# Kernel optimization log

Measured on AMD Instinct MI355X. Metric: run time of the kernel, lower is better.

## Reference

```python
import jax, jax.numpy as jnp
import numpy as np

B = 32; NMAX = 256; E = 512; H = 512; U = 256; M = 32; L = 2; P = 4; TAU = 1.0
S = NMAX + 1                      # pseudo-seq len = nodes + SOS
IN0 = E + (M - 1) + P             # GRU layer-0 input size


def setup_inputs() -> dict:
    key = jax.random.key(0)
    ks = jax.random.split(key, 22)
    f = lambda k, sh, sc=0.05: jax.random.normal(k, sh, dtype=jnp.float32) * sc
    return {
        "h_padded": jax.random.normal(ks[0], (B, NMAX, E), jnp.float32),
        "hg": jax.random.normal(ks[1], (B, E), jnp.float32),
        "num_nodes": jax.random.randint(ks[2], (B,), 1, NMAX + 1),
        "u_noise": jax.random.uniform(ks[3], (M, B, S), jnp.float32),
        "emb_special": f(ks[4], (2, E), 1.0),
        "emb_pos": f(ks[5], (M, P), 1.0),
        "Wp": f(ks[6], (L * H, E)), "bp": f(ks[7], (L * H,)),
        "W_ih0": f(ks[8], (3 * H, IN0)), "W_hh0": f(ks[9], (3 * H, H)),
        "b_ih0": f(ks[10], (3 * H,)), "b_hh0": f(ks[11], (3 * H,)),
        "W_ih1": f(ks[12], (3 * H, H)), "W_hh1": f(ks[13], (3 * H, H)),
        "b_ih1": f(ks[14], (3 * H,)), "b_hh1": f(ks[15], (3 * H,)),
        "W1": f(ks[16], (U, H)), "W2": f(ks[17], (U, H)),
        "wc": f(ks[18], (U,)), "V": f(ks[19], (U,)),
        "Wf": f(ks[20], (M - 1, H)), "bf": f(ks[21], (M - 1,)),
    }


def _gru_step(x, hid, params):
    # torch nn.GRU single time step, L layers; gate order (r, z, n)
    new = []
    inp = x
    for l, (Wi, Wh, bi, bh) in enumerate(params):
        hp = hid[l]
        gi = inp @ Wi.T + bi
        gh = hp @ Wh.T + bh
        gi_r, gi_z, gi_n = jnp.split(gi, 3, axis=-1)
        gh_r, gh_z, gh_n = jnp.split(gh, 3, axis=-1)
        r = jax.nn.sigmoid(gi_r + gh_r)
        z = jax.nn.sigmoid(gi_z + gh_z)
        n = jnp.tanh(gi_n + r * gh_n)
        hn = (1.0 - z) * n + z * hp
        new.append(hn)
        inp = hn
    return inp, jnp.stack(new, 0)


def reference(h_padded, hg, num_nodes, u_noise, emb_special, emb_pos, Wp, bp,
              W_ih0, W_hh0, b_ih0, b_hh0, W_ih1, W_hh1, b_ih1, b_hh1,
              W1, W2, wc, V, Wf, bf):
    lens = num_nodes + 1
    mask = jnp.arange(S)[None, :] < lens[:, None]                       # [B,S]
    node_valid = (jnp.arange(NMAX)[None, :] < num_nodes[:, None]).astype(h_padded.dtype)
    # encoder_out = [SOS emb ; h nodes ; zero pad] as pad_sequence would give
    sos_enc = jnp.broadcast_to(emb_special[1], (B, 1, E))
    encoder_out = jnp.concatenate([sos_enc, h_padded * node_valid[..., None]], axis=1)  # [B,S,E]
    enc_W1 = encoder_out @ W1.T                                          # [B,S,U] hoisted (loop-invariant)
    dec_hidden = jnp.tanh(hg @ Wp.T + bp).reshape(B, L, H).transpose(1, 0, 2)  # [L,B,H]
    theta0 = jnp.zeros((B, M - 1), encoder_out.dtype)
    dec_input = jnp.concatenate([jnp.broadcast_to(emb_special[0], (B, E)), theta0], axis=1)
    cov_vec0 = jnp.zeros((B, S), encoder_out.dtype)
    gumbel = -jnp.log(-jnp.log(u_noise + 1e-10) + 1e-10)                 # [M,B,S]
    gru_params = ((W_ih0, W_hh0, b_ih0, b_hh0), (W_ih1, W_hh1, b_ih1, b_hh1))
    neg = jnp.float32(-1e30)

    def step(carry, xs):
        dec_in, hid, cov_vec, cov_loss = carry
        i, pe, g = xs
        x = jnp.concatenate([dec_in, jnp.broadcast_to(pe, (B, P))], axis=1)
        out, hid = _gru_step(x, hid, gru_params)                        # out [B,H]
        # Bahdanau attention with coverage
        uj = enc_W1 + (out @ W2.T)[:, None, :] + cov_vec[..., None] * wc
        uj = jnp.tanh(uj) @ V                                           # [B,S]
        aj = jax.nn.softmax(jnp.where(mask, uj, neg), axis=-1)
        # hard gumbel-softmax (straight-through)
        logits = jnp.log(aj + 1e-12)
        y = jax.nn.softmax((logits + g) / TAU, axis=1)
        onehot = jax.nn.one_hot(jnp.argmax(y, axis=1), S, dtype=y.dtype)
        hard = jax.lax.stop_gradient(onehot - y) + y
        chosen = jnp.einsum('bse,bs->be', encoder_out, hard)            # [B,E]
        cov_loss = cov_loss + jnp.minimum(aj, cov_vec).sum()
        cov_vec = cov_vec + aj
        theta = jnp.where(i < 1,
                          jnp.zeros((B, M - 1), out.dtype),
                          jax.nn.sigmoid(out @ Wf.T + bf))
        dec_next = jnp.concatenate([chosen, theta], axis=1)
        return (dec_next, hid, cov_vec, cov_loss), (hard, theta, aj)

    init = (dec_input, dec_hidden, cov_vec0, jnp.float32(0.0))
    xs = (jnp.arange(M), emb_pos, gumbel)
    carry_f, (hards, thetas, ajs) = jax.lax.scan(step, init, xs)
    cov_loss = carry_f[3] / B
    pointer = jnp.transpose(hards, (1, 2, 0))   # [B,S,M]
    adj = jnp.transpose(thetas, (1, 2, 0))      # [B,M-1,M]
    atts = jnp.transpose(ajs, (1, 2, 0))        # [B,S,M]
    return pointer, cov_loss, encoder_out, adj, atts
```

## Files before the change

kernel.cpp:

```cpp
#include <hip/hip_runtime.h>

constexpr int NB  = 32;
constexpr int NMX = 256;
constexpr int ED  = 512;
constexpr int HD  = 512;
constexpr int UD  = 256;
constexpr int MS  = 32;
constexpr int PD  = 4;
constexpr int SD  = 257;
constexpr int IL0 = 547;
constexpr int XP  = 576;

constexpr long long OFF_PTR  = 0;
constexpr long long OFF_COVL = (long long)NB*SD*MS;
constexpr long long OFF_ENC  = OFF_COVL + 1;
constexpr long long OFF_ADJ  = OFF_ENC + (long long)NB*SD*ED;
constexpr long long OFF_ATT  = OFF_ADJ + (long long)NB*(MS-1)*MS;

__device__ __forceinline__ float sigf(float x){ return 1.0f/(1.0f + __expf(-x)); }
__device__ __forceinline__ float ftanh(float x){ float e = __expf(2.0f*x); return 1.0f - 2.0f/(e + 1.0f); }

__global__ __launch_bounds__(256) void k_pro(const float* __restrict__ hp,
    const float* __restrict__ hg, const float* __restrict__ embsp,
    const float* __restrict__ embpos, const float* __restrict__ W1,
    const float* __restrict__ Wih0, const float* __restrict__ W2,
    const int* __restrict__ nn, const float4* __restrict__ Wp4,
    const float* __restrict__ bp,
    float* __restrict__ out, float* __restrict__ encA, int useA,
    float4* __restrict__ encW1,
    float* __restrict__ x4, float* __restrict__ cov, float* __restrict__ covl,
    float* __restrict__ Wih0_4, float* __restrict__ W2T,
    float* __restrict__ h0, float* __restrict__ h1){
  __shared__ __align__(16) float As[16][68];
  __shared__ __align__(16) float Bs[16][68];
  int blk = blockIdx.x, t = threadIdx.x;
  if (blk < 516){
    int bm = blk >> 2, bn = blk & 3;
    int m0 = bm*64, n0 = bn*64;
    int tm = t >> 4, tn = t & 15;
    float4 acc[4];
    #pragma unroll
    for (int i = 0; i < 4; ++i) acc[i] = {0.f,0.f,0.f,0.f};
    int arow = t >> 2, akq = t & 3;
    int r = m0 + arow;
    int amode = 0;
    const float* abase = embsp + ED;
    if (r < NB*SD){
      int ab = r / SD, as = r - ab*SD;
      if (as == 0) amode = 1;
      else if (as <= nn[ab]){ amode = 2; abase = hp + ((long long)ab*NMX + (as-1))*ED; }
    }
    int bk = t & 15, bu = t >> 4;
    for (int k0 = 0; k0 < 512; k0 += 16){
      float4 av = {0.f,0.f,0.f,0.f};
      if (amode) av = *(const float4*)(abase + k0 + akq*4);
      float bv[4];
      #pragma unroll
      for (int j = 0; j < 4; ++j)
        bv[j] = W1[(long long)(n0 + bu*4 + j)*ED + k0 + bk];
      __syncthreads();
      As[akq*4 + 0][arow] = av.x;
      As[akq*4 + 1][arow] = av.y;
      As[akq*4 + 2][arow] = av.z;
      As[akq*4 + 3][arow] = av.w;
      *(float4*)&Bs[bk][bu*4] = make_float4(bv[0], bv[1], bv[2], bv[3]);
      __syncthreads();
      #pragma unroll
      for (int kk = 0; kk < 16; ++kk){
        float4 a = *(const float4*)&As[kk][tm*4];
        float4 bq = *(const float4*)&Bs[kk][tn*4];
        acc[0].x += a.x*bq.x; acc[0].y += a.x*bq.y; acc[0].z += a.x*bq.z; acc[0].w += a.x*bq.w;
        acc[1].x += a.y*bq.x; acc[1].y += a.y*bq.y; acc[1].z += a.y*bq.z; acc[1].w += a.y*bq.w;
        acc[2].x += a.z*bq.x; acc[2].y += a.z*bq.y; acc[2].z += a.z*bq.z; acc[2].w += a.z*bq.w;
        acc[3].x += a.w*bq.x; acc[3].y += a.w*bq.y; acc[3].z += a.w*bq.z; acc[3].w += a.w*bq.w;
      }
    }
    #pragma unroll
    for (int i = 0; i < 4; ++i){
      int rr = m0 + tm*4 + i;
      if (rr < NB*SD) encW1[(long long)rr*64 + (n0 >> 2) + tn] = acc[i];
    }
  } else if (blk < 644){
    int b = t & 31;
    int row = (blk - 516)*8 + (t >> 5);
    const float4* w = Wp4 + (long long)row*128;
    const float4* xg = (const float4*)(hg + (long long)b*ED);
    float acc = bp[row];
    #pragma unroll 4
    for (int i = 0; i < 128; ++i){
      float4 wv = w[i], xv = xg[i];
      acc += wv.x*xv.x + wv.y*xv.y + wv.z*xv.z + wv.w*xv.w;
    }
    float v = ftanh(acc);
    int h = row & 511;
    int idx = (h >> 2)*128 + b*4 + (h & 3);
    if (row < HD) h0[idx] = v;
    else          h1[idx] = v;
  } else {
    int eb = blk - 644;
    {
      int r = eb*2 + (t >> 7);
      int tid = t & 127;
      int b = r / SD, s = r - b*SD;
      float4 v = {0.f,0.f,0.f,0.f};
      if (s == 0) v = *(const float4*)(embsp + ED + tid*4);
      else if (s <= nn[b]) v = *(const float4*)(hp + ((long long)b*NMX + (s-1))*ED + tid*4);
      float* dst = out + OFF_ENC + (long long)r*ED + tid*4;
      dst[0] = v.x; dst[1] = v.y; dst[2] = v.z; dst[3] = v.w;
      if (useA) *(float4*)(encA + (long long)r*ED + tid*4) = v;
    }
    const int N0 = XP*NB;
    const int N1 = N0 + NB*SD;
    const int N2 = N1 + NB;
    const int N3 = N2 + 1536*XP;
    const int N4 = N3 + ED*UD;
    for (int i = eb*256 + t; i < N4; i += 4112*256){
      if (i < N0){
        int kb = i >> 7, rr = i & 3;
        int k = kb*4 + rr;
        float v;
        if (k < ED) v = embsp[k];
        else if (k < ED + MS - 1) v = 0.f;
        else if (k < IL0) v = embpos[k - (ED + MS - 1)];
        else v = 0.f;
        x4[i] = v;
      } else if (i < N1){
        cov[i - N0] = 0.f;
      } else if (i < N2){
        covl[i - N1] = 0.f;
      } else if (i < N3){
        int j = i - N2; int row = j / XP, c = j % XP;
        Wih0_4[j] = (c < IL0) ? Wih0[(long long)row*IL0 + c] : 0.f;
      } else {
        int j = i - N3; int k = j / UD, u = j % UD;
        W2T[j] = W2[(long long)u*HD + k];
      }
    }
  }
}

__device__ __forceinline__ void hh_pre(const float4* __restrict__ h4,
    const float4* __restrict__ Whh4, float* __restrict__ ghh,
    int bh, int t, float (*part)[NB][8][6]){
  int b = t & 31, ks = (t >> 5) & 7, hl = (t >> 8) & 1;
  int h = bh*2 + hl;
  float a0 = 0.f, a1 = 0.f, a2 = 0.f;
  const float4* w0 = Whh4 + (long long)(0*HD + h)*128 + ks*16;
  const float4* w1 = Whh4 + (long long)(1*HD + h)*128 + ks*16;
  const float4* w2 = Whh4 + (long long)(2*HD + h)*128 + ks*16;
  const float4* hb = h4 + (long long)(ks*16)*NB + b;
  #pragma unroll
  for (int kb = 0; kb < 16; ++kb){
    float4 xv = hb[kb*NB];
    float4 a = w0[kb], c = w1[kb], d = w2[kb];
    a0 += xv.x*a.x + xv.y*a.y + xv.z*a.z + xv.w*a.w;
    a1 += xv.x*c.x + xv.y*c.y + xv.z*c.z + xv.w*c.w;
    a2 += xv.x*d.x + xv.y*d.y + xv.z*d.z + xv.w*d.w;
  }
  part[hl][b][ks][0] = a0; part[hl][b][ks][1] = a1; part[hl][b][ks][2] = a2;
  __syncthreads();
  if (t < 64){
    int b2 = t & 31, hl2 = t >> 5;
    int h2 = bh*2 + hl2;
    float g0 = 0.f, g1 = 0.f, g2 = 0.f;
    #pragma unroll
    for (int k = 0; k < 8; ++k){
      g0 += part[hl2][b2][k][0]; g1 += part[hl2][b2][k][1]; g2 += part[hl2][b2][k][2];
    }
    ghh[(0*HD + h2)*NB + b2] = g0;
    ghh[(1*HD + h2)*NB + b2] = g1;
    ghh[(2*HD + h2)*NB + b2] = g2;
  }
}

template<int PER, bool PRE>
__global__ __launch_bounds__(512) void k_gru(const float4* __restrict__ x4,
                      const float4* __restrict__ h4,
                      const float4* __restrict__ Wih4, const float4* __restrict__ Whh4,
                      const float* __restrict__ bih, const float* __restrict__ bhh,
                      float* __restrict__ outT, const float* __restrict__ ghh){
  constexpr int NI4 = PER*8;
  __shared__ float part[2][NB][8][6];
  int t = threadIdx.x;
  int b = t & 31, ks = (t >> 5) & 7, hl = (t >> 8) & 1;
  int h = blockIdx.x*2 + hl;
  float ai0 = 0.f, ai1 = 0.f, ai2 = 0.f;
  {
    const float4* w0 = Wih4 + (long long)(0*HD + h)*NI4 + ks*PER;
    const float4* w1 = Wih4 + (long long)(1*HD + h)*NI4 + ks*PER;
    const float4* w2 = Wih4 + (long long)(2*HD + h)*NI4 + ks*PER;
    const float4* xb = x4 + (long long)(ks*PER)*NB + b;
    #pragma unroll
    for (int kb = 0; kb < PER; ++kb){
      float4 xv = xb[kb*NB];
      float4 a = w0[kb], c = w1[kb], d = w2[kb];
      ai0 += xv.x*a.x + xv.y*a.y + xv.z*a.z + xv.w*a.w;
      ai1 += xv.x*c.x + xv.y*c.y + xv.z*c.z + xv.w*c.w;
      ai2 += xv.x*d.x + xv.y*d.y + xv.z*d.z + xv.w*d.w;
    }
  }
  if (!PRE){
    float ah0 = 0.f, ah1 = 0.f, ah2 = 0.f;
    const float4* w0 = Whh4 + (long long)(0*HD + h)*128 + ks*16;
    const float4* w1 = Whh4 + (long long)(1*HD + h)*128 + ks*16;
    const float4* w2 = Whh4 + (long long)(2*HD + h)*128 + ks*16;
    const float4* hb = h4 + (long long)(ks*16)*NB + b;
    #pragma unroll
    for (int kb = 0; kb < 16; ++kb){
      float4 xv = hb[kb*NB];
      float4 a = w0[kb], c = w1[kb], d = w2[kb];
      ah0 += xv.x*a.x + xv.y*a.y + xv.z*a.z + xv.w*a.w;
      ah1 += xv.x*c.x + xv.y*c.y + xv.z*c.z + xv.w*c.w;
      ah2 += xv.x*d.x + xv.y*d.y + xv.z*d.z + xv.w*d.w;
    }
    part[hl][b][ks][3] = ah0; part[hl][b][ks][4] = ah1; part[hl][b][ks][5] = ah2;
  }
  part[hl][b][ks][0] = ai0; part[hl][b][ks][1] = ai1; part[hl][b][ks][2] = ai2;
  __syncthreads();
  if (t < 64){
    int b2 = t & 31, hl2 = t >> 5;
    int h2 = blockIdx.x*2 + hl2;
    float g0=0.f,g1=0.f,g2=0.f;
    #pragma unroll
    for (int k = 0; k < 8; ++k){
      g0 += part[hl2][b2][k][0]; g1 += part[hl2][b2][k][1]; g2 += part[hl2][b2][k][2];
    }
    float ghr, ghz, ghn;
    if (PRE){
      ghr = ghh[(0*HD + h2)*NB + b2];
      ghz = ghh[(1*HD + h2)*NB + b2];
      ghn = ghh[(2*HD + h2)*NB + b2];
    } else {
      float g3=0.f,g4=0.f,g5=0.f;
      #pragma unroll
      for (int k = 0; k < 8; ++k){
        g3 += part[hl2][b2][k][3]; g4 += part[hl2][b2][k][4]; g5 += part[hl2][b2][k][5];
      }
      ghr = g3; ghz = g4; ghn = g5;
    }
    float gir = g0 + bih[h2], giz = g1 + bih[HD + h2], gin = g2 + bih[2*HD + h2];
    ghr += bhh[h2]; ghz += bhh[HD + h2]; ghn += bhh[2*HD + h2];
    float r = sigf(gir + ghr);
    float z = sigf(giz + ghz);
    float nn = ftanh(gin + r*ghn);
    int idx = (h2 >> 2)*128 + b2*4 + (h2 & 3);
    float hp = ((const float*)h4)[idx];
    outT[idx] = (1.f - z)*nn + z*hp;
  }
}

__global__ __launch_bounds__(512) void k_qs(const float4* __restrict__ h1,
                      const float4* __restrict__ W2T4, const float4* __restrict__ Wf4,
                      const float* __restrict__ bfv, const float* __restrict__ embpos,
                      int m, const float4* __restrict__ encW1,
                      const float4* __restrict__ wc4, const float4* __restrict__ V4,
                      const int* __restrict__ nn,
                      const float* __restrict__ cov, float* __restrict__ sc,
                      float* __restrict__ x4, float* __restrict__ out,
                      const float4* __restrict__ Whh1_4, float* __restrict__ ghh1){
  union QMem {
    struct { float h1s[512]; float wcs[256]; float Vs[256]; float qs[256];
             float4 qpart[8][64]; } q;
    float part[2][NB][8][6];
  };
  __shared__ __align__(16) QMem sm;
  int t = threadIdx.x;
  if (blockIdx.x >= 256){
    hh_pre(h1, Whh1_4, ghh1, blockIdx.x - 256, t, sm.part);
    return;
  }
  int b = blockIdx.x >> 3, seg = blockIdx.x & 7;
  int n = nn[b];
  if (seg != 0 && seg*33 > n) return;
  if (t < 128) ((float4*)sm.q.h1s)[t] = h1[t*NB + b];
  else if (t < 192) ((float4*)sm.q.wcs)[t - 128] = wc4[t - 128];
  else if (t < 256) ((float4*)sm.q.Vs)[t - 192] = V4[t - 192];
  __syncthreads();
  {
    int u4 = t & 63, kq = t >> 6;
    float4 acc = {0.f,0.f,0.f,0.f};
    const float4* w = W2T4 + (long long)(kq*64)*64 + u4;
    const float* hh = sm.q.h1s + kq*64;
    #pragma unroll 4
    for (int k = 0; k < 64; ++k){
      float a = hh[k];
      float4 wv = w[(long long)k*64];
      acc.x += a*wv.x; acc.y += a*wv.y; acc.z += a*wv.z; acc.w += a*wv.w;
    }
    sm.q.qpart[kq][u4] = acc;
  }
  __syncthreads();
  if (t < 64){
    float4 s = sm.q.qpart[0][t];
    #pragma unroll
    for (int k = 1; k < 8; ++k){
      float4 p = sm.q.qpart[k][t];
      s.x += p.x; s.y += p.y; s.z += p.z; s.w += p.w;
    }
    ((float4*)sm.q.qs)[t] = s;
  } else if (seg == 0){
    int w = (t >> 6) - 1;
    int lane = t & 63;
    for (int j = w; j < MS-1; j += 7){
      const float4* wf = Wf4 + (long long)j*128 + lane*2;
      float4 w0 = wf[0], w1v = wf[1];
      const float4* hh4 = (const float4*)sm.q.h1s + lane*2;
      float4 hv0 = hh4[0], hv1 = hh4[1];
      float d = w0.x*hv0.x + w0.y*hv0.y + w0.z*hv0.z + w0.w*hv0.w
              + w1v.x*hv1.x + w1v.y*hv1.y + w1v.z*hv1.z + w1v.w*hv1.w;
      for (int off = 32; off; off >>= 1) d += __shfl_xor(d, off);
      if (lane == 0){
        float th = (m < 1) ? 0.f : sigf(d + bfv[j]);
        out[OFF_ADJ + (long long)b*(MS-1)*MS + (long long)j*MS + m] = th;
        int k = ED + j;
        x4[(k >> 2)*128 + b*4 + (k & 3)] = th;
      }
    }
  }
  if (seg == 0 && t == 0 && m + 1 < MS){
    #pragma unroll
    for (int p = 0; p < PD; ++p){
      int k = ED + MS - 1 + p;
      x4[(k >> 2)*128 + b*4 + (k & 3)] = embpos[(m+1)*PD + p];
    }
  }
  __syncthreads();
  int lane = t & 63, wav = t >> 6;
  int s0 = seg*33;
  float4 q4 = ((const float4*)sm.q.qs)[lane];
  float4 wv = ((const float4*)sm.q.wcs)[lane];
  float4 vv = ((const float4*)sm.q.Vs)[lane];
  for (int s = s0 + wav; s < s0 + 33 && s < SD; s += 8){
    if (s > n) continue;
    float cv = cov[b*SD + s];
    float4 e4 = encW1[((long long)b*SD + s)*64 + lane];
    float acc = vv.x*ftanh(e4.x + q4.x + cv*wv.x)
              + vv.y*ftanh(e4.y + q4.y + cv*wv.y)
              + vv.z*ftanh(e4.z + q4.z + cv*wv.z)
              + vv.w*ftanh(e4.w + q4.w + cv*wv.w);
    for (int off = 32; off; off >>= 1) acc += __shfl_xor(acc, off);
    if (lane == 0) sc[b*SD + s] = acc;
  }
}

__global__ __launch_bounds__(512) void k_soft(const float* __restrict__ sc,
                      const int* __restrict__ nn, const float* __restrict__ un, int m,
                      float* __restrict__ cov, float* __restrict__ covl,
                      float* __restrict__ out, float4* __restrict__ x4,
                      const float* __restrict__ encSrc, int alignedA,
                      const float4* __restrict__ h0n4,
                      const float4* __restrict__ Whh0_4, float* __restrict__ ghh0){
  union SMem {
    struct { float red[8]; float redc[8]; int redi[8]; float s_mx, s_den; int s_k; } s;
    float part[2][NB][8][6];
  };
  __shared__ __align__(16) SMem sm;
  int t = threadIdx.x;
  if (blockIdx.x >= 32){
    hh_pre(h0n4, Whh0_4, ghh0, blockIdx.x - 32, t, sm.part);
    return;
  }
  int b = blockIdx.x;
  int lane = t & 63, wav = t >> 6;
  int n = nn[b];
  float sv = (t < SD) ? sc[b*SD + t] : -3.4e38f;
  float cv = (t < SD) ? cov[b*SD + t] : 0.f;
  float v1 = (t < SD && t <= n) ? sv : -3.4e38f;
  for (int off = 32; off; off >>= 1) v1 = fmaxf(v1, __shfl_xor(v1, off));
  if (lane == 0) sm.s.red[wav] = v1;
  __syncthreads();
  if (t == 0){
    float mm = sm.s.red[0];
    for (int i = 1; i < 8; ++i) mm = fmaxf(mm, sm.s.red[i]);
    sm.s.s_mx = mm;
  }
  __syncthreads();
  float ev = (t < SD && t <= n) ? __expf(sv - sm.s.s_mx) : 0.f;
  float v2 = ev;
  for (int off = 32; off; off >>= 1) v2 += __shfl_xor(v2, off);
  if (lane == 0) sm.s.red[wav] = v2;
  __syncthreads();
  if (t == 0){
    float ss = 0.f;
    for (int i = 0; i < 8; ++i) ss += sm.s.red[i];
    sm.s.s_den = ss;
  }
  __syncthreads();
  float aj = (t < SD) ? ev / sm.s.s_den : 0.f;
  float yl = -3.4e38f; int idx = SD; float lcl = 0.f;
  if (t < SD){
    float u = un[((long long)m*NB + b)*SD + t];
    float g = -__logf(-__logf(u + 1e-10f) + 1e-10f);
    yl = __logf(aj + 1e-12f) + g;
    idx = t;
    lcl = fminf(aj, cv);
    cov[b*SD + t] = cv + aj;
    out[OFF_ATT + ((long long)b*SD + t)*MS + m] = aj;
  }
  for (int off = 32; off; off >>= 1){
    float oy = __shfl_xor(yl, off); int oi = __shfl_xor(idx, off);
    if (oy > yl || (oy == yl && oi < idx)){ yl = oy; idx = oi; }
  }
  for (int off = 32; off; off >>= 1) lcl += __shfl_xor(lcl, off);
  if (lane == 0){ sm.s.red[wav] = yl; sm.s.redi[wav] = idx; sm.s.redc[wav] = lcl; }
  __syncthreads();
  if (t == 0){
    float by = sm.s.red[0]; int bi = sm.s.redi[0]; float cl = sm.s.redc[0];
    for (int w = 1; w < 8; ++w){
      if (sm.s.red[w] > by || (sm.s.red[w] == by && sm.s.redi[w] < bi)){
        by = sm.s.red[w]; bi = sm.s.redi[w];
      }
      cl += sm.s.redc[w];
    }
    sm.s.s_k = bi;
    covl[b] += cl;
  }
  __syncthreads();
  int kk = sm.s.s_k;
  if (t < SD) out[OFF_PTR + ((long long)b*SD + t)*MS + m] = (t == kk) ? 1.f : 0.f;
  if (t < 128){
    if (alignedA){
      float4 v = ((const float4*)(encSrc + (long long)(b*SD + kk)*ED))[t];
      x4[t*NB + b] = v;
    } else {
      const float* er = encSrc + (long long)(b*SD + kk)*ED;
      float4 v; v.x = er[t*4]; v.y = er[t*4+1]; v.z = er[t*4+2]; v.w = er[t*4+3];
      x4[t*NB + b] = v;
    }
  }
}

__global__ void k_fin(const float* __restrict__ covl, float* __restrict__ out){
  if (threadIdx.x == 0 && blockIdx.x == 0){
    float s = 0.f;
    for (int i = 0; i < NB; ++i) s += covl[i];
    out[OFF_COVL] = s / (float)NB;
  }
}

extern "C" void kernel_launch(void* const* d_in, const int* in_sizes, int n_in,
                              void* d_out, int out_size, void* d_ws, size_t ws_size,
                              hipStream_t stream){
  const float* h_padded    = (const float*)d_in[0];
  const float* hg          = (const float*)d_in[1];
  const int*   num_nodes   = (const int*)  d_in[2];
  const float* u_noise     = (const float*)d_in[3];
  const float* emb_special = (const float*)d_in[4];
  const float* emb_pos     = (const float*)d_in[5];
  const float* Wp          = (const float*)d_in[6];
  const float* bp          = (const float*)d_in[7];
  const float* W_ih0       = (const float*)d_in[8];
  const float* W_hh0       = (const float*)d_in[9];
  const float* b_ih0       = (const float*)d_in[10];
  const float* b_hh0       = (const float*)d_in[11];
  const float* W_ih1       = (const float*)d_in[12];
  const float* W_hh1       = (const float*)d_in[13];
  const float* b_ih1       = (const float*)d_in[14];
  const float* b_hh1       = (const float*)d_in[15];
  const float* W1          = (const float*)d_in[16];
  const float* W2          = (const float*)d_in[17];
  const float* wc          = (const float*)d_in[18];
  const float* V           = (const float*)d_in[19];
  const float* Wf          = (const float*)d_in[20];
  const float* bf          = (const float*)d_in[21];
  float* out = (float*)d_out;

  float* ws      = (float*)d_ws;
  float* encW1   = ws;  ws += (long long)NB*SD*UD;
  float* Wih0_4  = ws;  ws += (long long)1536*XP;
  float* W2T     = ws;  ws += (long long)UD*ED;
  float* x4      = ws;  ws += XP*NB;
  float* h0      = ws;  ws += 2*HD*NB;
  float* h1      = ws;  ws += 2*HD*NB;
  float* cov     = ws;  ws += NB*SD;
  float* covl    = ws;  ws += NB;
  float* sc      = ws;  ws += NB*SD;
  float* ghh0    = ws;  ws += 3*HD*NB;
  float* ghh1    = ws;  ws += 3*HD*NB;
  float* encA    = ws;
  size_t used_base = (size_t)((char*)ws - (char*)d_ws);
  int useA = (ws_size >= used_base + (size_t)NB*SD*ED*sizeof(float)) ? 1 : 0;
  const float* encSrc = useA ? encA : (out + OFF_ENC);

  k_pro<<<4756, 256, 0, stream>>>(h_padded, hg, emb_special, emb_pos, W1, W_ih0, W2,
                                  num_nodes, (const float4*)Wp, bp, out, encA, useA,
                                  (float4*)encW1, x4, cov, covl, Wih0_4, W2T, h0, h1);

  for (int m = 0; m < MS; ++m){
    float* h0c = h0 + (m & 1)*HD*NB;
    float* h0n = h0 + ((m + 1) & 1)*HD*NB;
    float* h1c = h1 + (m & 1)*HD*NB;
    float* h1n = h1 + ((m + 1) & 1)*HD*NB;
    if (m == 0){
      k_gru<18,false><<<256, 512, 0, stream>>>((const float4*)x4, (const float4*)h0c,
          (const float4*)Wih0_4, (const float4*)W_hh0, b_ih0, b_hh0, h0n, nullptr);
      k_gru<16,false><<<256, 512, 0, stream>>>((const float4*)h0n, (const float4*)h1c,
          (const float4*)W_ih1, (const float4*)W_hh1, b_ih1, b_hh1, h1n, nullptr);
    } else {
      k_gru<18,true><<<256, 512, 0, stream>>>((const float4*)x4, (const float4*)h0c,
          (const float4*)Wih0_4, (const float4*)W_hh0, b_ih0, b_hh0, h0n, ghh0);
      k_gru<16,true><<<256, 512, 0, stream>>>((const float4*)h0n, (const float4*)h1c,
          (const float4*)W_ih1, (const float4*)W_hh1, b_ih1, b_hh1, h1n, ghh1);
    }
    k_qs  <<<512, 512, 0, stream>>>((const float4*)h1n, (const float4*)W2T,
        (const float4*)Wf, bf, emb_pos, m, (const float4*)encW1,
        (const float4*)wc, (const float4*)V, num_nodes, cov, sc, x4, out,
        (const float4*)W_hh1, ghh1);
    k_soft<<<288, 512, 0, stream>>>(sc, num_nodes, u_noise, m, cov, covl, out,
        (float4*)x4, encSrc, useA, (const float4*)h0n, (const float4*)W_hh0, ghh0);
  }
  k_fin<<<1, 64, 0, stream>>>(covl, out);
}
```

Baseline: 1.219 ms.

## Fuse attention scoring and gumbel-softmax into one kernel per decode step

```diff
diff --git a/kernel.cpp b/kernel.cpp
--- a/kernel.cpp
+++ b/kernel.cpp
@@ -28,7 +28,7 @@
     const float* __restrict__ bp,
     float* __restrict__ out, float* __restrict__ encA, int useA,
     float4* __restrict__ encW1,
-    float* __restrict__ x4, float* __restrict__ cov, float* __restrict__ covl,
+    float* __restrict__ x4, float* __restrict__ cov2, float* __restrict__ covp,
     float* __restrict__ Wih0_4, float* __restrict__ W2T,
     float* __restrict__ h0, float* __restrict__ h1){
   __shared__ __align__(16) float As[16][68];
@@ -110,8 +110,8 @@
       if (useA) *(float4*)(encA + (long long)r*ED + tid*4) = v;
     }
     const int N0 = XP*NB;
-    const int N1 = N0 + NB*SD;
-    const int N2 = N1 + NB;
+    const int N1 = N0 + 2*NB*SD;
+    const int N2 = N1 + 256;
     const int N3 = N2 + 1536*XP;
     const int N4 = N3 + ED*UD;
     for (int i = eb*256 + t; i < N4; i += 4112*256){
@@ -125,9 +125,9 @@
         else v = 0.f;
         x4[i] = v;
       } else if (i < N1){
-        cov[i - N0] = 0.f;
+        cov2[i - N0] = 0.f;
       } else if (i < N2){
-        covl[i - N1] = 0.f;
+        covp[i - N1] = 0.f;
       } else if (i < N3){
         int j = i - N2; int row = j / XP, c = j % XP;
         Wih0_4[j] = (c < IL0) ? Wih0[(long long)row*IL0 + c] : 0.f;
@@ -249,62 +249,78 @@
   }
 }
 
-__global__ __launch_bounds__(512) void k_qs(const float4* __restrict__ h1,
+union __align__(16) AMem {
+  struct { __align__(16) float h1s[512]; __align__(16) float wcs[256];
+           __align__(16) float Vs[256];  __align__(16) float qs[256];
+           __align__(16) float4 qpart[8][64]; float scs[SD];
+           float red[8]; float redc[8]; int redi[8];
+           float s_mx, s_den; int s_k; } a;
+  float part[2][NB][8][6];
+};
+
+__global__ __launch_bounds__(512) void k_attn(const float4* __restrict__ h1,
                       const float4* __restrict__ W2T4, const float4* __restrict__ Wf4,
                       const float* __restrict__ bfv, const float* __restrict__ embpos,
                       int m, const float4* __restrict__ encW1,
                       const float4* __restrict__ wc4, const float4* __restrict__ V4,
-                      const int* __restrict__ nn,
-                      const float* __restrict__ cov, float* __restrict__ sc,
-                      float* __restrict__ x4, float* __restrict__ out,
+                      const int* __restrict__ nn, const float* __restrict__ un,
+                      const float* __restrict__ covc, float* __restrict__ covn,
+                      float* __restrict__ covp, float* __restrict__ x4,
+                      float* __restrict__ out, const float* __restrict__ encSrc,
+                      int alignedA,
+                      const float4* __restrict__ h0n4,
+                      const float4* __restrict__ Whh0_4, float* __restrict__ ghh0,
                       const float4* __restrict__ Whh1_4, float* __restrict__ ghh1){
-  union QMem {
-    struct { float h1s[512]; float wcs[256]; float Vs[256]; float qs[256];
-             float4 qpart[8][64]; } q;
-    float part[2][NB][8][6];
-  };
-  __shared__ __align__(16) QMem sm;
+  __shared__ AMem sm;
   int t = threadIdx.x;
-  if (blockIdx.x >= 256){
-    hh_pre(h1, Whh1_4, ghh1, blockIdx.x - 256, t, sm.part);
-    return;
-  }
+  if (blockIdx.x >= 512){ hh_pre(h0n4, Whh0_4, ghh0, blockIdx.x - 512, t, sm.part); return; }
+  if (blockIdx.x >= 256){ hh_pre(h1,   Whh1_4, ghh1, blockIdx.x - 256, t, sm.part); return; }
   int b = blockIdx.x >> 3, seg = blockIdx.x & 7;
   int n = nn[b];
-  if (seg != 0 && seg*33 > n) return;
-  if (t < 128) ((float4*)sm.q.h1s)[t] = h1[t*NB + b];
-  else if (t < 192) ((float4*)sm.q.wcs)[t - 128] = wc4[t - 128];
-  else if (t < 256) ((float4*)sm.q.Vs)[t - 192] = V4[t - 192];
+  int s0 = seg*33;
+  if (seg != 0 && s0 > n){
+    if (t < 33){
+      int s = s0 + t;
+      if (s < SD){
+        out[OFF_ATT + ((long long)b*SD + s)*MS + m] = 0.f;
+        out[OFF_PTR + ((long long)b*SD + s)*MS + m] = 0.f;
+      }
+    }
+    return;
+  }
+  if (t < 128) ((float4*)sm.a.h1s)[t] = h1[t*NB + b];
+  else if (t < 192) ((float4*)sm.a.wcs)[t - 128] = wc4[t - 128];
+  else if (t < 256) ((float4*)sm.a.Vs)[t - 192] = V4[t - 192];
   __syncthreads();
   {
     int u4 = t & 63, kq = t >> 6;
     float4 acc = {0.f,0.f,0.f,0.f};
     const float4* w = W2T4 + (long long)(kq*64)*64 + u4;
-    const float* hh = sm.q.h1s + kq*64;
+    const float* hh = sm.a.h1s + kq*64;
     #pragma unroll 4
     for (int k = 0; k < 64; ++k){
       float a = hh[k];
       float4 wv = w[(long long)k*64];
       acc.x += a*wv.x; acc.y += a*wv.y; acc.z += a*wv.z; acc.w += a*wv.w;
     }
-    sm.q.qpart[kq][u4] = acc;
+    sm.a.qpart[kq][u4] = acc;
   }
   __syncthreads();
   if (t < 64){
-    float4 s = sm.q.qpart[0][t];
+    float4 s = sm.a.qpart[0][t];
     #pragma unroll
     for (int k = 1; k < 8; ++k){
-      float4 p = sm.q.qpart[k][t];
+      float4 p = sm.a.qpart[k][t];
       s.x += p.x; s.y += p.y; s.z += p.z; s.w += p.w;
     }
-    ((float4*)sm.q.qs)[t] = s;
+    ((float4*)sm.a.qs)[t] = s;
   } else if (seg == 0){
     int w = (t >> 6) - 1;
     int lane = t & 63;
     for (int j = w; j < MS-1; j += 7){
       const float4* wf = Wf4 + (long long)j*128 + lane*2;
       float4 w0 = wf[0], w1v = wf[1];
-      const float4* hh4 = (const float4*)sm.q.h1s + lane*2;
+      const float4* hh4 = (const float4*)sm.a.h1s + lane*2;
       float4 hv0 = hh4[0], hv1 = hh4[1];
       float d = w0.x*hv0.x + w0.y*hv0.y + w0.z*hv0.z + w0.w*hv0.w
               + w1v.x*hv1.x + w1v.y*hv1.y + w1v.z*hv1.z + w1v.w*hv1.w;
@@ -325,117 +341,104 @@
     }
   }
   __syncthreads();
+  {
+    int lane = t & 63, wav = t >> 6;
+    float4 q4 = ((const float4*)sm.a.qs)[lane];
+    float4 wv = ((const float4*)sm.a.wcs)[lane];
+    float4 vv = ((const float4*)sm.a.Vs)[lane];
+    for (int s = wav; s < SD; s += 8){
+      if (s > n) continue;
+      float cv2 = covc[b*SD + s];
+      float4 e4 = encW1[((long long)b*SD + s)*64 + lane];
+      float acc = vv.x*ftanh(e4.x + q4.x + cv2*wv.x)
+                + vv.y*ftanh(e4.y + q4.y + cv2*wv.y)
+                + vv.z*ftanh(e4.z + q4.z + cv2*wv.z)
+                + vv.w*ftanh(e4.w + q4.w + cv2*wv.w);
+      for (int off = 32; off; off >>= 1) acc += __shfl_xor(acc, off);
+      if (lane == 0) sm.a.scs[s] = acc;
+    }
+  }
+  __syncthreads();
   int lane = t & 63, wav = t >> 6;
-  int s0 = seg*33;
-  float4 q4 = ((const float4*)sm.q.qs)[lane];
-  float4 wv = ((const float4*)sm.q.wcs)[lane];
-  float4 vv = ((const float4*)sm.q.Vs)[lane];
-  for (int s = s0 + wav; s < s0 + 33 && s < SD; s += 8){
-    if (s > n) continue;
-    float cv = cov[b*SD + s];
-    float4 e4 = encW1[((long long)b*SD + s)*64 + lane];
-    float acc = vv.x*ftanh(e4.x + q4.x + cv*wv.x)
-              + vv.y*ftanh(e4.y + q4.y + cv*wv.y)
-              + vv.z*ftanh(e4.z + q4.z + cv*wv.z)
-              + vv.w*ftanh(e4.w + q4.w + cv*wv.w);
-    for (int off = 32; off; off >>= 1) acc += __shfl_xor(acc, off);
-    if (lane == 0) sc[b*SD + s] = acc;
-  }
-}
-
-__global__ __launch_bounds__(512) void k_soft(const float* __restrict__ sc,
-                      const int* __restrict__ nn, const float* __restrict__ un, int m,
-                      float* __restrict__ cov, float* __restrict__ covl,
-                      float* __restrict__ out, float4* __restrict__ x4,
-                      const float* __restrict__ encSrc, int alignedA,
-                      const float4* __restrict__ h0n4,
-                      const float4* __restrict__ Whh0_4, float* __restrict__ ghh0){
-  union SMem {
-    struct { float red[8]; float redc[8]; int redi[8]; float s_mx, s_den; int s_k; } s;
-    float part[2][NB][8][6];
-  };
-  __shared__ __align__(16) SMem sm;
-  int t = threadIdx.x;
-  if (blockIdx.x >= 32){
-    hh_pre(h0n4, Whh0_4, ghh0, blockIdx.x - 32, t, sm.part);
-    return;
-  }
-  int b = blockIdx.x;
-  int lane = t & 63, wav = t >> 6;
-  int n = nn[b];
-  float sv = (t < SD) ? sc[b*SD + t] : -3.4e38f;
-  float cv = (t < SD) ? cov[b*SD + t] : 0.f;
-  float v1 = (t < SD && t <= n) ? sv : -3.4e38f;
+  float sv = (t < SD && t <= n) ? sm.a.scs[t] : -3.4e38f;
+  float cv = (t < SD) ? covc[b*SD + t] : 0.f;
+  float v1 = sv;
   for (int off = 32; off; off >>= 1) v1 = fmaxf(v1, __shfl_xor(v1, off));
-  if (lane == 0) sm.s.red[wav] = v1;
+  if (lane == 0) sm.a.red[wav] = v1;
   __syncthreads();
   if (t == 0){
-    float mm = sm.s.red[0];
-    for (int i = 1; i < 8; ++i) mm = fmaxf(mm, sm.s.red[i]);
-    sm.s.s_mx = mm;
-  }
-  __syncthreads();
-  float ev = (t < SD && t <= n) ? __expf(sv - sm.s.s_mx) : 0.f;
+    float mm = sm.a.red[0];
+    for (int i = 1; i < 8; ++i) mm = fmaxf(mm, sm.a.red[i]);
+    sm.a.s_mx = mm;
+  }
+  __syncthreads();
+  float ev = (t < SD && t <= n) ? __expf(sv - sm.a.s_mx) : 0.f;
   float v2 = ev;
   for (int off = 32; off; off >>= 1) v2 += __shfl_xor(v2, off);
-  if (lane == 0) sm.s.red[wav] = v2;
+  if (lane == 0) sm.a.red[wav] = v2;
   __syncthreads();
   if (t == 0){
     float ss = 0.f;
-    for (int i = 0; i < 8; ++i) ss += sm.s.red[i];
-    sm.s.s_den = ss;
-  }
-  __syncthreads();
-  float aj = (t < SD) ? ev / sm.s.s_den : 0.f;
-  float yl = -3.4e38f; int idx = SD; float lcl = 0.f;
+    for (int i = 0; i < 8; ++i) ss += sm.a.red[i];
+    sm.a.s_den = ss;
+  }
+  __syncthreads();
+  float aj = (t < SD) ? ev / sm.a.s_den : 0.f;
+  float yl = -3.4e38f; int idx = SD;
   if (t < SD){
     float u = un[((long long)m*NB + b)*SD + t];
     float g = -__logf(-__logf(u + 1e-10f) + 1e-10f);
     yl = __logf(aj + 1e-12f) + g;
     idx = t;
+  }
+  bool own = (t >= s0) && (t < s0 + 33) && (t < SD);
+  float lcl = 0.f;
+  if (own){
+    out[OFF_ATT + ((long long)b*SD + t)*MS + m] = aj;
+    covn[b*SD + t] = cv + aj;
     lcl = fminf(aj, cv);
-    cov[b*SD + t] = cv + aj;
-    out[OFF_ATT + ((long long)b*SD + t)*MS + m] = aj;
   }
   for (int off = 32; off; off >>= 1){
     float oy = __shfl_xor(yl, off); int oi = __shfl_xor(idx, off);
     if (oy > yl || (oy == yl && oi < idx)){ yl = oy; idx = oi; }
   }
   for (int off = 32; off; off >>= 1) lcl += __shfl_xor(lcl, off);
-  if (lane == 0){ sm.s.red[wav] = yl; sm.s.redi[wav] = idx; sm.s.redc[wav] = lcl; }
+  if (lane == 0){ sm.a.red[wav] = yl; sm.a.redi[wav] = idx; sm.a.redc[wav] = lcl; }
   __syncthreads();
   if (t == 0){
-    float by = sm.s.red[0]; int bi = sm.s.redi[0]; float cl = sm.s.redc[0];
+    float by = sm.a.red[0]; int bi = sm.a.redi[0]; float cl = sm.a.redc[0];
     for (int w = 1; w < 8; ++w){
-      if (sm.s.red[w] > by || (sm.s.red[w] == by && sm.s.redi[w] < bi)){
-        by = sm.s.red[w]; bi = sm.s.redi[w];
+      if (sm.a.red[w] > by || (sm.a.red[w] == by && sm.a.redi[w] < bi)){
+        by = sm.a.red[w]; bi = sm.a.redi[w];
       }
-      cl += sm.s.redc[w];
-    }
-    sm.s.s_k = bi;
-    covl[b] += cl;
-  }
-  __syncthreads();
-  int kk = sm.s.s_k;
-  if (t < SD) out[OFF_PTR + ((long long)b*SD + t)*MS + m] = (t == kk) ? 1.f : 0.f;
-  if (t < 128){
+      cl += sm.a.redc[w];
+    }
+    sm.a.s_k = bi;
+    covp[b*8 + seg] += cl;
+  }
+  __syncthreads();
+  int kk = sm.a.s_k;
+  if (own) out[OFF_PTR + ((long long)b*SD + t)*MS + m] = (t == kk) ? 1.f : 0.f;
+  if (seg == 0 && t < 128){
     if (alignedA){
       float4 v = ((const float4*)(encSrc + (long long)(b*SD + kk)*ED))[t];
-      x4[t*NB + b] = v;
+      ((float4*)x4)[t*NB + b] = v;
     } else {
       const float* er = encSrc + (long long)(b*SD + kk)*ED;
       float4 v; v.x = er[t*4]; v.y = er[t*4+1]; v.z = er[t*4+2]; v.w = er[t*4+3];
-      x4[t*NB + b] = v;
+      ((float4*)x4)[t*NB + b] = v;
     }
   }
 }
 
-__global__ void k_fin(const float* __restrict__ covl, float* __restrict__ out){
-  if (threadIdx.x == 0 && blockIdx.x == 0){
-    float s = 0.f;
-    for (int i = 0; i < NB; ++i) s += covl[i];
-    out[OFF_COVL] = s / (float)NB;
-  }
+__global__ void k_fin(const float* __restrict__ covp, float* __restrict__ out){
+  __shared__ float r4[4];
+  int t = threadIdx.x;
+  float v = covp[t];
+  for (int off = 32; off; off >>= 1) v += __shfl_xor(v, off);
+  if ((t & 63) == 0) r4[t >> 6] = v;
+  __syncthreads();
+  if (t == 0) out[OFF_COVL] = (r4[0] + r4[1] + r4[2] + r4[3]) / (float)NB;
 }
 
 extern "C" void kernel_launch(void* const* d_in, const int* in_sizes, int n_in,
@@ -472,9 +475,8 @@
   float* x4      = ws;  ws += XP*NB;
   float* h0      = ws;  ws += 2*HD*NB;
   float* h1      = ws;  ws += 2*HD*NB;
-  float* cov     = ws;  ws += NB*SD;
-  float* covl    = ws;  ws += NB;
-  float* sc      = ws;  ws += NB*SD;
+  float* cov2    = ws;  ws += 2*NB*SD;
+  float* covp    = ws;  ws += 256;
   float* ghh0    = ws;  ws += 3*HD*NB;
   float* ghh1    = ws;  ws += 3*HD*NB;
   float* encA    = ws;
@@ -484,13 +486,15 @@
 
   k_pro<<<4756, 256, 0, stream>>>(h_padded, hg, emb_special, emb_pos, W1, W_ih0, W2,
                                   num_nodes, (const float4*)Wp, bp, out, encA, useA,
-                                  (float4*)encW1, x4, cov, covl, Wih0_4, W2T, h0, h1);
+                                  (float4*)encW1, x4, cov2, covp, Wih0_4, W2T, h0, h1);
 
   for (int m = 0; m < MS; ++m){
     float* h0c = h0 + (m & 1)*HD*NB;
     float* h0n = h0 + ((m + 1) & 1)*HD*NB;
     float* h1c = h1 + (m & 1)*HD*NB;
     float* h1n = h1 + ((m + 1) & 1)*HD*NB;
+    float* covc = cov2 + (m & 1)*NB*SD;
+    float* covn = cov2 + ((m + 1) & 1)*NB*SD;
     if (m == 0){
       k_gru<18,false><<<256, 512, 0, stream>>>((const float4*)x4, (const float4*)h0c,
           (const float4*)Wih0_4, (const float4*)W_hh0, b_ih0, b_hh0, h0n, nullptr);
@@ -502,12 +506,12 @@
       k_gru<16,true><<<256, 512, 0, stream>>>((const float4*)h0n, (const float4*)h1c,
           (const float4*)W_ih1, (const float4*)W_hh1, b_ih1, b_hh1, h1n, ghh1);
     }
-    k_qs  <<<512, 512, 0, stream>>>((const float4*)h1n, (const float4*)W2T,
+    k_attn<<<768, 512, 0, stream>>>((const float4*)h1n, (const float4*)W2T,
         (const float4*)Wf, bf, emb_pos, m, (const float4*)encW1,
-        (const float4*)wc, (const float4*)V, num_nodes, cov, sc, x4, out,
+        (const float4*)wc, (const float4*)V, num_nodes, u_noise,
+        covc, covn, covp, x4, out, encSrc, useA,
+        (const float4*)h0n, (const float4*)W_hh0, ghh0,
         (const float4*)W_hh1, ghh1);
-    k_soft<<<288, 512, 0, stream>>>(sc, num_nodes, u_noise, m, cov, covl, out,
-        (float4*)x4, encSrc, useA, (const float4*)h0n, (const float4*)W_hh0, ghh0);
-  }
-  k_fin<<<1, 64, 0, stream>>>(covl, out);
+  }
+  k_fin<<<1, 256, 0, stream>>>(covp, out);
 }
```

New measurement: 1.769 ms. +45.1%, slower.
